# Optimization experiments

Measured on AMD Instinct MI355X. Metric: run time of the kernel, lower is better.

The kernel has to match this reference:

```python
import jax, jax.numpy as jnp
import numpy as np

BATCH, T, ALPHABET, N_STATES = 64, 4096, 32, 128


def setup_inputs() -> dict:
    key = jax.random.key(0)
    k1, k2, k3, k4 = jax.random.split(key, 4)
    # one-hot emission sequences (DNA-style categorical observations)
    tokens = jax.random.randint(k1, (BATCH, T), 0, ALPHABET)
    inputs = jax.nn.one_hot(tokens, ALPHABET, dtype=jnp.float32)  # [B, T, A]
    A_logits = jax.random.normal(k2, (N_STATES, N_STATES), dtype=jnp.float32)
    B_logits = jax.random.normal(k3, (ALPHABET, N_STATES), dtype=jnp.float32)
    I_logits = jax.random.normal(k4, (N_STATES,), dtype=jnp.float32)
    return {"inputs": inputs, "A_logits": A_logits, "B_logits": B_logits, "I_logits": I_logits}


def reference(inputs, A_logits, B_logits, I_logits):
    # Softmax-parameterized HMM: rows of A sum to 1 (transitions), columns of B
    # sum to 1 over the alphabet (emissions per state), I is the initial dist.
    A = jax.nn.softmax(A_logits, axis=1)          # [S, S]
    Bm = jax.nn.softmax(B_logits, axis=0)          # [A, S]
    I = jax.nn.softmax(I_logits)                   # [S]

    # Per-step emission likelihoods for every state (batched lookup via one-hot matmul)
    E = jnp.einsum('bta,as->bts', inputs, Bm)      # [B, T, S]

    # t = 0: alpha_0 = I * E_0, normalized; loglik accumulates the scale factors
    alpha = I[None, :] * E[:, 0]                   # [B, S]
    s = jnp.sum(alpha, axis=1, keepdims=True)      # [B, 1]
    alpha = alpha / s
    loglik = jnp.log(s[:, 0])                      # [B]

    def step(carry, Et):
        alpha, loglik = carry
        alpha = jnp.matmul(alpha, A) * Et          # [B, S]
        s = jnp.sum(alpha, axis=1, keepdims=True)
        alpha = alpha / s
        loglik = loglik + jnp.log(s[:, 0])
        return (alpha, loglik), None

    E_rest = jnp.swapaxes(E[:, 1:], 0, 1)          # time-major [T-1, B, S]
    (alpha, loglik), _ = jax.lax.scan(step, (alpha, loglik), E_rest)
    return loglik                                   # loglik_state, shape [B]
```

## Files before the change

### kernel.cpp

```cpp
#include <hip/hip_runtime.h>
#include <math.h>

#define BATCH 64
#define T 4096
#define ALPH 32
#define NS 128
#define MB 16
#define NGRP (BATCH / MB)
#define NCHUNK 256
#define CL (T / NCHUNK)
#define WARM 16

typedef __bf16 bf16x8 __attribute__((ext_vector_type(8)));
typedef short  short8 __attribute__((ext_vector_type(8)));
typedef float  f32x4  __attribute__((ext_vector_type(4)));

#define WS_ABF 0
#define WS_BM 8192
#define WS_I 12288
#define WS_TOK_F 12416

static __device__ inline short f2s(float f) {
    __bf16 b = (__bf16)f;
    return __builtin_bit_cast(short, b);
}

__global__ __launch_bounds__(256) void setup_kernel(const float* __restrict__ onehot,
                                                    const float* __restrict__ A_logits,
                                                    const float* __restrict__ B_logits,
                                                    const float* __restrict__ I_logits,
                                                    float* __restrict__ ws,
                                                    float* __restrict__ out,
                                                    unsigned char* __restrict__ tok) {
    unsigned short* A_bf = (unsigned short*)(ws + WS_ABF);
    float* Bm_ws = ws + WS_BM;
    float* I_ws  = ws + WS_I;
    const int blk = blockIdx.x;
    const int tid = threadIdx.x;

    if (blk < 1024) {
        int b = blk >> 4;
        int t = (blk & 15) * 256 + tid;
        const float4* p = (const float4*)(onehot + ((size_t)b * T + t) * ALPH);
        int tk = 0;
        #pragma unroll
        for (int q = 0; q < 8; ++q) {
            float4 v = p[q];
            if (v.x > 0.5f) tk = 4 * q + 0;
            if (v.y > 0.5f) tk = 4 * q + 1;
            if (v.z > 0.5f) tk = 4 * q + 2;
            if (v.w > 0.5f) tk = 4 * q + 3;
        }
        tok[(size_t)b * T + t] = (unsigned char)tk;
        return;
    }

    if (blk == 1024 + NS + 1) {
        if (tid < NS) {
            int s = tid;
            float m = -1e30f;
            for (int a = 0; a < ALPH; ++a) m = fmaxf(m, B_logits[a * NS + s]);
            float sum = 0.f;
            for (int a = 0; a < ALPH; ++a) sum += expf(B_logits[a * NS + s] - m);
            float inv = 1.0f / sum;
            for (int a = 0; a < ALPH; ++a)
                Bm_ws[a * NS + s] = expf(B_logits[a * NS + s] - m) * inv;
        } else if (tid < NS + BATCH) {
            out[tid - NS] = 0.0f;
        }
        return;
    }

    int row = blk - 1024;
    const float* src = (row < NS) ? (A_logits + row * NS) : I_logits;
    __shared__ float redm[4];
    __shared__ float reds[4];
    float x = (tid < NS) ? src[tid] : -1e30f;
    float m = x;
    #pragma unroll
    for (int off = 1; off < 64; off <<= 1) m = fmaxf(m, __shfl_xor(m, off));
    int wid = tid >> 6;
    if ((tid & 63) == 0) redm[wid] = m;
    __syncthreads();
    m = fmaxf(fmaxf(redm[0], redm[1]), fmaxf(redm[2], redm[3]));
    float e = (tid < NS) ? expf(x - m) : 0.0f;
    float sg = e;
    #pragma unroll
    for (int off = 1; off < 64; off <<= 1) sg += __shfl_xor(sg, off);
    if ((tid & 63) == 0) reds[wid] = sg;
    __syncthreads();
    float total = (reds[0] + reds[1]) + (reds[2] + reds[3]);
    float v = e / total;
    if (tid < NS) {
        if (row < NS) A_bf[row * NS + tid] = (unsigned short)f2s(v);
        else          I_ws[tid] = v;
    }
}

__global__ __launch_bounds__(256) void hmm_kernel(const float* __restrict__ ws,
                                                  const unsigned char* __restrict__ tok_g,
                                                  float* __restrict__ out) {
    const unsigned short* A_bf = (const unsigned short*)(ws + WS_ABF);
    const float* Bm_g = ws + WS_BM;
    const float* I_ws = ws + WS_I;

    const int g = blockIdx.x;
    const int c = blockIdx.y;
    const int tid  = threadIdx.x;
    const int w    = tid >> 6;
    const int lane = tid & 63;
    const int quad = lane >> 4;
    const int col  = lane & 15;
    const int nbase = w * 32;

    __shared__ float Bm_lds[ALPH * 129];
    __shared__ __align__(16) short alpha_lds[2][MB * 136];
    __shared__ unsigned char tok_lds[(CL + WARM + 1) * MB];

    const int t0     = (c == 0) ? 0 : (c * CL - WARM);
    const int nsteps = (c == 0) ? (CL - 1) : (CL + WARM - 1);
    const int ntok   = nsteps + 1;
    const int resetj = (c == 0) ? -1 : WARM;

    for (int i = tid; i < ALPH * NS; i += 256)
        Bm_lds[(i >> 7) * 129 + (i & 127)] = Bm_g[i];
    for (int i = tid; i < ntok * MB; i += 256) {
        int m = i & (MB - 1);
        int t = i >> 4;
        tok_lds[i] = tok_g[(size_t)(g * MB + m) * T + t0 + t];
    }

    bf16x8 bfr[4][2];
    #pragma unroll
    for (int kc = 0; kc < 4; ++kc) {
        #pragma unroll
        for (int nt = 0; nt < 2; ++nt) {
            short8 bs;
            #pragma unroll
            for (int j = 0; j < 8; ++j)
                bs[j] = (short)A_bf[(kc * 32 + quad * 8 + j) * NS + nbase + nt * 16 + col];
            bfr[kc][nt] = __builtin_bit_cast(bf16x8, bs);
        }
    }

    __syncthreads();

    {
        int m = tid >> 4;
        int seg = tid & 15;
        int tk0 = tok_lds[m];
        #pragma unroll
        for (int kk = 0; kk < 8; ++kk) {
            int k = seg * 8 + kk;
            float val = (c == 0) ? (I_ws[k] * Bm_lds[tk0 * 129 + k]) : 1.0f;
            alpha_lds[0][m * 136 + k] = f2s(val);
        }
    }
    __syncthreads();

    float loglik = 0.0f;

    for (int j = 1; j <= nsteps; ++j) {
        const int rb = (j + 1) & 1;
        const int wb = j & 1;
        const bool do_norm = ((j & 7) == 0);

        unsigned tokp = *(const unsigned*)&tok_lds[j * MB + quad * 4];
        float e0[4], e1[4];
        #pragma unroll
        for (int r = 0; r < 4; ++r) {
            int tk = (tokp >> (8 * r)) & 255;
            e0[r] = Bm_lds[tk * 129 + nbase + col];
            e1[r] = Bm_lds[tk * 129 + nbase + 16 + col];
        }

        const short* ap = &alpha_lds[rb][col * 136 + quad * 8];
        bf16x8 afr[4];
        #pragma unroll
        for (int kc = 0; kc < 4; ++kc)
            afr[kc] = *(const bf16x8*)(ap + kc * 32);

        f32x4 acc0 = {0.f, 0.f, 0.f, 0.f};
        f32x4 acc1 = {0.f, 0.f, 0.f, 0.f};
        #pragma unroll
        for (int kc = 0; kc < 4; ++kc) {
            acc0 = __builtin_amdgcn_mfma_f32_16x16x32_bf16(afr[kc], bfr[kc][0], acc0, 0, 0, 0);
            acc1 = __builtin_amdgcn_mfma_f32_16x16x32_bf16(afr[kc], bfr[kc][1], acc1, 0, 0, 0);
        }

        float v0[4], v1[4];
        #pragma unroll
        for (int r = 0; r < 4; ++r) {
            v0[r] = acc0[r] * e0[r];
            v1[r] = acc1[r] * e1[r];
        }

        if (do_norm) {
            float asum = 0.f;
            #pragma unroll
            for (int kc = 0; kc < 4; ++kc) {
                #pragma unroll
                for (int jj = 0; jj < 8; ++jj) asum += (float)afr[kc][jj];
            }
            asum += __shfl_xor(asum, 16);
            asum += __shfl_xor(asum, 32);
            float lg = __logf(asum);
            loglik = (j == resetj) ? 0.0f : (loglik + lg);
            float inv = __builtin_amdgcn_rcpf(asum);
            #pragma unroll
            for (int r = 0; r < 4; ++r) { v0[r] *= inv; v1[r] *= inv; }
        }

        #pragma unroll
        for (int r = 0; r < 4; ++r) {
            int row = (quad * 4 + r) * 136;
            alpha_lds[wb][row + nbase + col]      = f2s(v0[r]);
            alpha_lds[wb][row + nbase + 16 + col] = f2s(v1[r]);
        }
        __syncthreads();
    }

    {
        const short* ap = &alpha_lds[nsteps & 1][col * 136 + quad * 8];
        float tot = 0.f;
        #pragma unroll
        for (int kc = 0; kc < 4; ++kc) {
            bf16x8 av = *(const bf16x8*)(ap + kc * 32);
            #pragma unroll
            for (int jj = 0; jj < 8; ++jj) tot += (float)av[jj];
        }
        tot += __shfl_xor(tot, 16);
        tot += __shfl_xor(tot, 32);
        if (w == 0 && quad == 0)
            atomicAdd(out + g * MB + col, loglik + __logf(tot));
    }
}

extern "C" void kernel_launch(void* const* d_in, const int* in_sizes, int n_in,
                              void* d_out, int out_size, void* d_ws, size_t ws_size,
                              hipStream_t stream) {
    const float* onehot   = (const float*)d_in[0];
    const float* A_logits = (const float*)d_in[1];
    const float* B_logits = (const float*)d_in[2];
    const float* I_logits = (const float*)d_in[3];
    float* ws  = (float*)d_ws;
    float* out = (float*)d_out;
    unsigned char* tok = (unsigned char*)(ws + WS_TOK_F);

    setup_kernel<<<dim3(1024 + NS + 2), dim3(256), 0, stream>>>(
        onehot, A_logits, B_logits, I_logits, ws, out, tok);
    hmm_kernel<<<dim3(NGRP, NCHUNK), dim3(256), 0, stream>>>(ws, tok, out);
}
```

Before: 111.6 us.

## Give each wave an independent batch group and remove per-step block barriers

The time-chunked HMM kernel now assigns one 16-sequence batch group to each wave of a block, and each wave computes all 128 output states itself. The full transition matrix is held in registers as fragments pre-swizzled in setup. Because every wave reads and writes only its own alpha buffers, the per-step __syncthreads is removed, and emissions are stored in bf16 in a layout matching the MFMA outputs. The atomicAdd accumulation is replaced by per-chunk partial writes followed by a small reduce kernel. In exchange, each wave issues four times as many MFMAs per step and needs many more registers (launch bounds 256,1), and the grid drops to 256 blocks.

```diff
diff --git a/kernel.cpp b/kernel.cpp
--- a/kernel.cpp
+++ b/kernel.cpp
@@ -6,35 +6,36 @@
 #define ALPH 32
 #define NS 128
 #define MB 16
-#define NGRP (BATCH / MB)
+#define NGRP 4
 #define NCHUNK 256
-#define CL (T / NCHUNK)
+#define CL 16
 #define WARM 16
 
 typedef __bf16 bf16x8 __attribute__((ext_vector_type(8)));
 typedef short  short8 __attribute__((ext_vector_type(8)));
 typedef float  f32x4  __attribute__((ext_vector_type(4)));
 
-#define WS_ABF 0
-#define WS_BM 8192
-#define WS_I 12288
-#define WS_TOK_F 12416
-
-static __device__ inline short f2s(float f) {
+#define WS_FRAG 0
+#define WS_BME  8192
+#define WS_I    10240
+#define WS_PART 10368
+#define WS_TOK_F 26752
+
+static __device__ inline unsigned short f2u(float f) {
     __bf16 b = (__bf16)f;
-    return __builtin_bit_cast(short, b);
-}
+    return __builtin_bit_cast(unsigned short, b);
+}
+
 
 __global__ __launch_bounds__(256) void setup_kernel(const float* __restrict__ onehot,
                                                     const float* __restrict__ A_logits,
                                                     const float* __restrict__ B_logits,
                                                     const float* __restrict__ I_logits,
                                                     float* __restrict__ ws,
-                                                    float* __restrict__ out,
                                                     unsigned char* __restrict__ tok) {
-    unsigned short* A_bf = (unsigned short*)(ws + WS_ABF);
-    float* Bm_ws = ws + WS_BM;
-    float* I_ws  = ws + WS_I;
+    unsigned short* frag = (unsigned short*)(ws + WS_FRAG);
+    unsigned short* Bme  = (unsigned short*)(ws + WS_BME);
+    float* I_ws = ws + WS_I;
     const int blk = blockIdx.x;
     const int tid = threadIdx.x;
 
@@ -55,7 +56,7 @@
         return;
     }
 
-    if (blk == 1024 + NS + 1) {
+    if (blk == 1024 + NS) {
         if (tid < NS) {
             int s = tid;
             float m = -1e30f;
@@ -63,19 +64,39 @@
             float sum = 0.f;
             for (int a = 0; a < ALPH; ++a) sum += expf(B_logits[a * NS + s] - m);
             float inv = 1.0f / sum;
+            int idx = (s & 15) * 8 + (s >> 4);
             for (int a = 0; a < ALPH; ++a)
-                Bm_ws[a * NS + s] = expf(B_logits[a * NS + s] - m) * inv;
-        } else if (tid < NS + BATCH) {
-            out[tid - NS] = 0.0f;
+                Bme[a * NS + idx] = f2u(expf(B_logits[a * NS + s] - m) * inv);
+        }
+        __shared__ float redm[4];
+        __shared__ float reds[4];
+        float x = (tid < NS) ? I_logits[tid] : -1e30f;
+        float m = x;
+        #pragma unroll
+        for (int off = 1; off < 64; off <<= 1) m = fmaxf(m, __shfl_xor(m, off));
+        int wid = tid >> 6;
+        if ((tid & 63) == 0) redm[wid] = m;
+        __syncthreads();
+        m = fmaxf(fmaxf(redm[0], redm[1]), fmaxf(redm[2], redm[3]));
+        float e = (tid < NS) ? expf(x - m) : 0.0f;
+        float sg = e;
+        #pragma unroll
+        for (int off = 1; off < 64; off <<= 1) sg += __shfl_xor(sg, off);
+        if ((tid & 63) == 0) reds[wid] = sg;
+        __syncthreads();
+        float total = (reds[0] + reds[1]) + (reds[2] + reds[3]);
+        if (tid < NS) {
+            int n = tid;
+            int p = (n >> 5) * 32 + (n & 15) * 2 + ((n >> 4) & 1);
+            I_ws[p] = e / total;
         }
         return;
     }
 
-    int row = blk - 1024;
-    const float* src = (row < NS) ? (A_logits + row * NS) : I_logits;
+    int rho = blk - 1024;
     __shared__ float redm[4];
     __shared__ float reds[4];
-    float x = (tid < NS) ? src[tid] : -1e30f;
+    float x = (tid < NS) ? A_logits[rho * NS + tid] : -1e30f;
     float m = x;
     #pragma unroll
     for (int off = 1; off < 64; off <<= 1) m = fmaxf(m, __shfl_xor(m, off));
@@ -90,73 +111,87 @@
     if ((tid & 63) == 0) reds[wid] = sg;
     __syncthreads();
     float total = (reds[0] + reds[1]) + (reds[2] + reds[3]);
-    float v = e / total;
     if (tid < NS) {
-        if (row < NS) A_bf[row * NS + tid] = (unsigned short)f2s(v);
-        else          I_ws[tid] = v;
-    }
-}
-
-__global__ __launch_bounds__(256) void hmm_kernel(const float* __restrict__ ws,
-                                                  const unsigned char* __restrict__ tok_g,
-                                                  float* __restrict__ out) {
-    const unsigned short* A_bf = (const unsigned short*)(ws + WS_ABF);
-    const float* Bm_g = ws + WS_BM;
+        float v = e / total;
+        int gamma = tid;
+        int kc   = rho >> 5;
+        int jlow = (rho >> 4) & 1;
+        int quad = (rho >> 2) & 3;
+        int j    = (rho & 3) * 2 + jlow;
+        int nt   = gamma >> 4;
+        int col  = gamma & 15;
+        int lane = quad * 16 + col;
+        int fid  = kc * 8 + nt;
+        frag[fid * 512 + lane * 8 + j] = f2u(v);
+    }
+}
+
+__global__ __launch_bounds__(256, 1) void hmm_kernel(const float* __restrict__ ws,
+                                                     const unsigned char* __restrict__ tok_g,
+                                                     float* __restrict__ part) {
+    const unsigned short* Bme_g = (const unsigned short*)(ws + WS_BME);
     const float* I_ws = ws + WS_I;
-
-    const int g = blockIdx.x;
-    const int c = blockIdx.y;
+    const char* frag_g = (const char*)(ws + WS_FRAG);
+
+    const int c    = blockIdx.x;
     const int tid  = threadIdx.x;
-    const int w    = tid >> 6;
+    const int g    = tid >> 6;
     const int lane = tid & 63;
     const int quad = lane >> 4;
     const int col  = lane & 15;
-    const int nbase = w * 32;
-
-    __shared__ float Bm_lds[ALPH * 129];
-    __shared__ __align__(16) short alpha_lds[2][MB * 136];
-    __shared__ unsigned char tok_lds[(CL + WARM + 1) * MB];
+
+    __shared__ unsigned short Bme_lds[ALPH * NS];
+    __shared__ __align__(16) short alpha_lds[NGRP][2][MB * 136];
+    __shared__ unsigned char tok_lds[(CL + WARM) * BATCH];
 
     const int t0     = (c == 0) ? 0 : (c * CL - WARM);
     const int nsteps = (c == 0) ? (CL - 1) : (CL + WARM - 1);
     const int ntok   = nsteps + 1;
     const int resetj = (c == 0) ? -1 : WARM;
 
-    for (int i = tid; i < ALPH * NS; i += 256)
-        Bm_lds[(i >> 7) * 129 + (i & 127)] = Bm_g[i];
-    for (int i = tid; i < ntok * MB; i += 256) {
-        int m = i & (MB - 1);
-        int t = i >> 4;
-        tok_lds[i] = tok_g[(size_t)(g * MB + m) * T + t0 + t];
-    }
-
-    bf16x8 bfr[4][2];
+    {
+        const unsigned* src = (const unsigned*)Bme_g;
+        unsigned* dst = (unsigned*)Bme_lds;
+        #pragma unroll
+        for (int i = 0; i < 8; ++i) dst[i * 256 + tid] = src[i * 256 + tid];
+    }
+    {
+        int b = tid & 63, half = tid >> 6;
+        if (half * 8 < ntok) {
+            uint2 v = *(const uint2*)(tok_g + (size_t)b * T + t0 + half * 8);
+            unsigned lo = v.x, hi = v.y;
+            #pragma unroll
+            for (int i = 0; i < 4; ++i) {
+                tok_lds[(half * 8 + i) * 64 + b]     = (unsigned char)((lo >> (8 * i)) & 255);
+                tok_lds[(half * 8 + 4 + i) * 64 + b] = (unsigned char)((hi >> (8 * i)) & 255);
+            }
+        }
+    }
+    bf16x8 bfr[32];
     #pragma unroll
-    for (int kc = 0; kc < 4; ++kc) {
-        #pragma unroll
-        for (int nt = 0; nt < 2; ++nt) {
-            short8 bs;
-            #pragma unroll
-            for (int j = 0; j < 8; ++j)
-                bs[j] = (short)A_bf[(kc * 32 + quad * 8 + j) * NS + nbase + nt * 16 + col];
-            bfr[kc][nt] = __builtin_bit_cast(bf16x8, bs);
-        }
-    }
+    for (int fid = 0; fid < 32; ++fid)
+        bfr[fid] = __builtin_bit_cast(bf16x8, *(const short8*)(frag_g + fid * 1024 + lane * 16));
 
     __syncthreads();
 
     {
-        int m = tid >> 4;
-        int seg = tid & 15;
-        int tk0 = tok_lds[m];
-        #pragma unroll
-        for (int kk = 0; kk < 8; ++kk) {
-            int k = seg * 8 + kk;
-            float val = (c == 0) ? (I_ws[k] * Bm_lds[tk0 * 129 + k]) : 1.0f;
-            alpha_lds[0][m * 136 + k] = f2s(val);
-        }
-    }
-    __syncthreads();
+        #pragma unroll
+        for (int it = 0; it < 32; ++it) {
+            int idx = it * 64 + lane;
+            int m = idx >> 7, p = idx & 127;
+            float val;
+            if (c == 0) {
+                int tk0 = tok_lds[0 * 64 + g * 16 + m];
+                int nt = ((p >> 5) << 1) + (p & 1);
+                int cc = (p >> 1) & 15;
+                float bm = (float)__builtin_bit_cast(__bf16, Bme_lds[tk0 * NS + cc * 8 + nt]);
+                val = I_ws[p] * bm;
+            } else {
+                val = 1.0f;
+            }
+            alpha_lds[g][0][m * 136 + p] = (short)f2u(val);
+        }
+    }
 
     float loglik = 0.0f;
 
@@ -165,36 +200,31 @@
         const int wb = j & 1;
         const bool do_norm = ((j & 7) == 0);
 
-        unsigned tokp = *(const unsigned*)&tok_lds[j * MB + quad * 4];
-        float e0[4], e1[4];
+        unsigned tokp = *(const unsigned*)&tok_lds[j * 64 + g * 16 + quad * 4];
+        bf16x8 efr[4];
         #pragma unroll
         for (int r = 0; r < 4; ++r) {
             int tk = (tokp >> (8 * r)) & 255;
-            e0[r] = Bm_lds[tk * 129 + nbase + col];
-            e1[r] = Bm_lds[tk * 129 + nbase + 16 + col];
-        }
-
-        const short* ap = &alpha_lds[rb][col * 136 + quad * 8];
+            efr[r] = *(const bf16x8*)&Bme_lds[tk * NS + col * 8];
+        }
+
+        const short* ap = &alpha_lds[g][rb][col * 136 + quad * 8];
         bf16x8 afr[4];
         #pragma unroll
         for (int kc = 0; kc < 4; ++kc)
             afr[kc] = *(const bf16x8*)(ap + kc * 32);
 
-        f32x4 acc0 = {0.f, 0.f, 0.f, 0.f};
-        f32x4 acc1 = {0.f, 0.f, 0.f, 0.f};
-        #pragma unroll
-        for (int kc = 0; kc < 4; ++kc) {
-            acc0 = __builtin_amdgcn_mfma_f32_16x16x32_bf16(afr[kc], bfr[kc][0], acc0, 0, 0, 0);
-            acc1 = __builtin_amdgcn_mfma_f32_16x16x32_bf16(afr[kc], bfr[kc][1], acc1, 0, 0, 0);
-        }
-
-        float v0[4], v1[4];
-        #pragma unroll
-        for (int r = 0; r < 4; ++r) {
-            v0[r] = acc0[r] * e0[r];
-            v1[r] = acc1[r] * e1[r];
-        }
-
+        f32x4 acc[8];
+        #pragma unroll
+        for (int nt = 0; nt < 8; ++nt) acc[nt] = (f32x4){0.f, 0.f, 0.f, 0.f};
+        #pragma unroll
+        for (int nt = 0; nt < 8; ++nt) {
+            #pragma unroll
+            for (int kc = 0; kc < 4; ++kc)
+                acc[nt] = __builtin_amdgcn_mfma_f32_16x16x32_bf16(afr[kc], bfr[kc * 8 + nt], acc[nt], 0, 0, 0);
+        }
+
+        float inv[4] = {1.0f, 1.0f, 1.0f, 1.0f};
         if (do_norm) {
             float asum = 0.f;
             #pragma unroll
@@ -206,22 +236,25 @@
             asum += __shfl_xor(asum, 32);
             float lg = __logf(asum);
             loglik = (j == resetj) ? 0.0f : (loglik + lg);
-            float inv = __builtin_amdgcn_rcpf(asum);
-            #pragma unroll
-            for (int r = 0; r < 4; ++r) { v0[r] *= inv; v1[r] *= inv; }
+            #pragma unroll
+            for (int r = 0; r < 4; ++r)
+                inv[r] = __builtin_amdgcn_rcpf(__shfl(asum, quad * 4 + r));
         }
 
         #pragma unroll
         for (int r = 0; r < 4; ++r) {
-            int row = (quad * 4 + r) * 136;
-            alpha_lds[wb][row + nbase + col]      = f2s(v0[r]);
-            alpha_lds[wb][row + nbase + 16 + col] = f2s(v1[r]);
-        }
-        __syncthreads();
+            unsigned* wrow = (unsigned*)&alpha_lds[g][wb][(quad * 4 + r) * 136];
+            #pragma unroll
+            for (int a = 0; a < 4; ++a) {
+                float x0 = acc[2 * a][r]     * (float)efr[r][2 * a]     * inv[r];
+                float x1 = acc[2 * a + 1][r] * (float)efr[r][2 * a + 1] * inv[r];
+                wrow[a * 16 + col] = (unsigned)f2u(x0) | ((unsigned)f2u(x1) << 16);
+            }
+        }
     }
 
     {
-        const short* ap = &alpha_lds[nsteps & 1][col * 136 + quad * 8];
+        const short* ap = &alpha_lds[g][nsteps & 1][col * 136 + quad * 8];
         float tot = 0.f;
         #pragma unroll
         for (int kc = 0; kc < 4; ++kc) {
@@ -231,9 +264,25 @@
         }
         tot += __shfl_xor(tot, 16);
         tot += __shfl_xor(tot, 32);
-        if (w == 0 && quad == 0)
-            atomicAdd(out + g * MB + col, loglik + __logf(tot));
-    }
+        if (quad == 0)
+            part[c * 64 + g * 16 + col] = loglik + __logf(tot);
+    }
+}
+
+__global__ __launch_bounds__(256) void reduce_kernel(const float* __restrict__ part,
+                                                     float* __restrict__ out) {
+    __shared__ float red[4][64];
+    int b = threadIdx.x & 63;
+    int cg = threadIdx.x >> 6;
+    float s = 0.f;
+    #pragma unroll 4
+    for (int k = 0; k < 64; ++k)
+        s += part[(cg * 64 + k) * 64 + b];
+    red[cg][b] = s;
+    __syncthreads();
+    if (threadIdx.x < 64)
+        out[threadIdx.x] = (red[0][threadIdx.x] + red[1][threadIdx.x]) +
+                           (red[2][threadIdx.x] + red[3][threadIdx.x]);
 }
 
 extern "C" void kernel_launch(void* const* d_in, const int* in_sizes, int n_in,
@@ -247,7 +296,8 @@
     float* out = (float*)d_out;
     unsigned char* tok = (unsigned char*)(ws + WS_TOK_F);
 
-    setup_kernel<<<dim3(1024 + NS + 2), dim3(256), 0, stream>>>(
-        onehot, A_logits, B_logits, I_logits, ws, out, tok);
-    hmm_kernel<<<dim3(NGRP, NCHUNK), dim3(256), 0, stream>>>(ws, tok, out);
-}
+    setup_kernel<<<dim3(1024 + NS + 1), dim3(256), 0, stream>>>(
+        onehot, A_logits, B_logits, I_logits, ws, tok);
+    hmm_kernel<<<dim3(NCHUNK), dim3(256), 0, stream>>>(ws, tok, ws + WS_PART);
+    reduce_kernel<<<dim3(1), dim3(256), 0, stream>>>(ws + WS_PART, out);
+}
```

After: 114.1 us. 1.02x slower.
